# Optimization experiments

Measured on AMD Instinct MI355X. Metric: run time of the kernel, lower is better.

The kernel has to match this reference:

```python
import jax, jax.numpy as jnp
import numpy as np

N = 20000
E = 640000
D = 128
NORM_FACTOR = 100.0
LN_EPS = 1e-5


def _layer_norm(x, g, b):
    mu = jnp.mean(x, axis=-1, keepdims=True)
    var = jnp.var(x, axis=-1, keepdims=True)
    return (x - mu) * jax.lax.rsqrt(var + LN_EPS) * g + b


def setup_inputs() -> dict:
    key = jax.random.key(0)
    ks = jax.random.split(key, 16)

    def lin(k, fan_in, shape):
        bound = 1.0 / np.sqrt(fan_in)
        return jax.random.uniform(k, shape, jnp.float32, -bound, bound)

    h = jax.random.normal(ks[0], (N, D), jnp.float32)
    distances = jax.random.uniform(ks[1], (E, 1), jnp.float32)
    edges = jax.random.randint(ks[2], (2, E), 0, N, jnp.int64)
    node_mask = jnp.ones((N, 1), jnp.float32)
    edge_mask = jnp.ones((E, 1), jnp.float32)

    return {
        "h": h, "distances": distances, "node_mask": node_mask, "edge_mask": edge_mask,
        # linear: in->out
        "lin_w": lin(ks[3], D, (D, D)), "lin_b": lin(ks[4], D, (D,)),
        # att_mlp: (2D+1)->2D -> 2D->D -> D->1
        "att_w1": lin(ks[5], 2 * D + 1, (2 * D, 2 * D + 1)), "att_b1": lin(ks[5], 2 * D + 1, (2 * D,)),
        "att_w2": lin(ks[6], 2 * D, (D, 2 * D)), "att_b2": lin(ks[6], 2 * D, (D,)),
        "att_w3": lin(ks[7], D, (1, D)), "att_b3": lin(ks[7], D, (1,)),
        # node_mlp: D->D, LN, SiLU, D->D
        "nm_w1": lin(ks[8], D, (D, D)), "nm_b1": lin(ks[8], D, (D,)),
        "nm_ln_g": jnp.ones((D,), jnp.float32), "nm_ln_b": jnp.zeros((D,), jnp.float32),
        "nm_w2": lin(ks[9], D, (D, D)), "nm_b2": lin(ks[9], D, (D,)),
        # final LayerNorm
        "ln_g": jnp.ones((D,), jnp.float32), "ln_b": jnp.zeros((D,), jnp.float32),
        "edges": edges,
    }


def reference(h, distances, node_mask, edge_mask,
              lin_w, lin_b, att_w1, att_b1, att_w2, att_b2, att_w3, att_b3,
              nm_w1, nm_b1, nm_ln_g, nm_ln_b, nm_w2, nm_b2, ln_g, ln_b, edges):
    x = h @ lin_w.T + lin_b                                  # [N, D]
    row, col = edges[0], edges[1]
    x_row = x[row]                                           # [E, D]
    x_col = x[col]                                           # [E, D]

    # DenseAtt
    d = distances * edge_mask
    x_cat = jnp.concatenate([x_row, x_col, d], axis=1)       # [E, 2D+1]
    a = jax.nn.silu(x_cat @ att_w1.T + att_b1)
    a = jax.nn.silu(a @ att_w2.T + att_b2)
    att = jax.nn.sigmoid(a @ att_w3.T + att_b3) * edge_mask  # [E, 1]

    agg = x_col * att                                        # [E, D]
    out = jax.ops.segment_sum(agg, row, num_segments=N) / NORM_FACTOR

    # node_mlp + residual
    o = out @ nm_w1.T + nm_b1
    o = jax.nn.silu(_layer_norm(o, nm_ln_g, nm_ln_b))
    o = o @ nm_w2.T + nm_b2
    hh = o + x

    hh = _layer_norm(hh, ln_g, ln_b)
    hh = jax.nn.silu(hh)                                     # act = SiLU
    return hh
```

## Files before the change

### kernel.cpp

```cpp
#include <hip/hip_runtime.h>
#include <hip/hip_bf16.h>

#define N_NODES 20000
#define E_EDGES 640000
#define DIM 128
#define CAP 96
#define EPB 64
#define NPB 8
#define XST 264

typedef __attribute__((ext_vector_type(8))) short bf16x8;
typedef __attribute__((ext_vector_type(4))) float f32x4;
typedef __attribute__((ext_vector_type(2))) float f32x2;
typedef __attribute__((ext_vector_type(4))) unsigned u32x4;

#define LOG2E 1.44269504f
__device__ __forceinline__ float fsilu(float x) {
    return x * __builtin_amdgcn_rcpf(1.f + __builtin_amdgcn_exp2f(-LOG2E * x));
}
__device__ __forceinline__ float fsig(float x) {
    return __builtin_amdgcn_rcpf(1.f + __builtin_amdgcn_exp2f(-LOG2E * x));
}
__device__ __forceinline__ f32x2 fsilu2(f32x2 v) {
    f32x2 m = v * (-LOG2E);
    f32x2 e; e.x = __builtin_amdgcn_exp2f(m.x); e.y = __builtin_amdgcn_exp2f(m.y);
    f32x2 den = e + 1.0f;
    f32x2 r; r.x = __builtin_amdgcn_rcpf(den.x); r.y = __builtin_amdgcn_rcpf(den.y);
    return v * r;
}

__device__ __forceinline__ unsigned short f2bf(float x) {
    union { float f; unsigned u; } v; v.f = x;
    unsigned r = (v.u + 0x7fffu + ((v.u >> 16) & 1u)) >> 16;
    return (unsigned short)r;
}
__device__ __forceinline__ float bf2f(unsigned short s) {
    union { unsigned u; float f; } v; v.u = ((unsigned)s) << 16;
    return v.f;
}
__device__ __forceinline__ unsigned pack_bf16(float lo, float hi) {
    union { float f; unsigned u; } a, b; a.f = lo; b.f = hi;
    unsigned ul = a.u + 0x8000u, uh = b.u + 0x8000u;
    return __builtin_amdgcn_perm(uh, ul, 0x07060302u);
}

#define PRE_PREP_BLOCKS 64
#define PRE_LIN_BLOCKS  625
#define PRE_CNT_BLOCKS  2500
__global__ __launch_bounds__(256) void pre_kernel(
    const float* __restrict__ w1, const float* __restrict__ w2,
    unsigned short* __restrict__ w1b, float* __restrict__ w1p,
    unsigned short* __restrict__ w2b,
    const float* __restrict__ h, const float* __restrict__ lw,
    const float* __restrict__ lb, float* __restrict__ x,
    unsigned short* __restrict__ xb,
    const int* __restrict__ edges, int* __restrict__ cnt, int E) {
    __shared__ float hs[32][128];
    int b = blockIdx.x;
    int t = threadIdx.x;

    if (b < PRE_PREP_BLOCKS) {
        int i = b * 256 + t;
        const int stride = PRE_PREP_BLOCKS * 256;
        for (int idx = i; idx < 256 * 256; idx += stride) {
            int o = idx >> 8, k = idx & 255;
            w1b[idx] = f2bf(w1[o * 257 + k]);
        }
        for (int idx = i; idx < 128 * 256; idx += stride) {
            int n2 = idx >> 8, p = idx & 255;
            int bb = p & ~31, off = p & 31;
            int ksrc = bb + (off >> 1) + ((off & 1) << 4);
            w2b[idx] = f2bf(w2[n2 * 256 + ksrc]);
        }
        for (int idx = i; idx < 256; idx += stride) {
            int bb = idx & ~31, off = idx & 31;
            int ksrc = bb + (off >> 1) + ((off & 1) << 4);
            w1p[idx] = w1[ksrc * 257 + 256];
        }
    } else if (b < PRE_PREP_BLOCKS + PRE_LIN_BLOCKS) {
        int nb = b - PRE_PREP_BLOCKS;
        int n0 = nb * 32;
        int ch = t & 127, g = t >> 7;
#pragma unroll
        for (int j = 0; j < 16; ++j) hs[g * 16 + j][ch] = h[(size_t)(n0 + g * 16 + j) * DIM + ch];
        __syncthreads();
        float acc[16];
#pragma unroll
        for (int j = 0; j < 16; ++j) acc[j] = 0.f;
        for (int kc = 0; kc < 128; kc += 4) {
            float4 wv = *(const float4*)&lw[(size_t)ch * DIM + kc];
#pragma unroll
            for (int j = 0; j < 16; ++j) {
                float4 hv = *(const float4*)&hs[g * 16 + j][kc];
                acc[j] += wv.x * hv.x + wv.y * hv.y + wv.z * hv.z + wv.w * hv.w;
            }
        }
        float bias = lb[ch];
#pragma unroll
        for (int j = 0; j < 16; ++j) {
            float v = acc[j] + bias;
            int n = n0 + g * 16 + j;
            x[(size_t)n * DIM + ch] = v;
            xb[(size_t)n * DIM + ch] = f2bf(v);
        }
    } else {
        int e = (b - PRE_PREP_BLOCKS - PRE_LIN_BLOCKS) * 256 + t;
        if (e < E) atomicAdd(&cnt[edges[e]], 1);
    }
}

__global__ __launch_bounds__(1024) void scan_kernel(const int* __restrict__ cnt,
                                                    int* __restrict__ off) {
    __shared__ int wsum[16], wbase[16];
    int t = threadIdx.x;
    int lane = t & 63, wid = t >> 6;
    int base = t * 20;
    int loc[20];
    int s = 0;
#pragma unroll
    for (int i = 0; i < 20; ++i) {
        int idx = base + i;
        int v = 0;
        if (idx < N_NODES) { v = cnt[idx]; v = v > CAP ? CAP : v; }
        loc[i] = s; s += v;
    }
    int inc = s;
#pragma unroll
    for (int d = 1; d < 64; d <<= 1) {
        int u = __shfl_up(inc, d);
        if (lane >= d) inc += u;
    }
    if (lane == 63) wsum[wid] = inc;
    __syncthreads();
    if (t < 16) {
        int v = wsum[t];
        int inc2 = v;
#pragma unroll
        for (int d = 1; d < 16; d <<= 1) {
            int u = __shfl_up(inc2, d);
            if (t >= d) inc2 += u;
        }
        wbase[t] = inc2 - v;
        if (t == 15) off[N_NODES] = inc2;
    }
    __syncthreads();
    int ex = wbase[wid] + inc - s;
#pragma unroll
    for (int i = 0; i < 20; ++i) {
        int idx = base + i;
        if (idx < N_NODES) off[idx] = ex + loc[i];
    }
}

#define MID_PRC_BLOCKS 1250
#define MID_SCAT_BLOCKS 2500
__global__ __launch_bounds__(256) void mid_kernel(
    const unsigned short* __restrict__ xb,
    const unsigned short* __restrict__ w1b,
    const float* __restrict__ b1,
    unsigned short* __restrict__ prb, unsigned short* __restrict__ pcb,
    const int* __restrict__ edges,
    const float* __restrict__ dist, const float* __restrict__ emask,
    int* __restrict__ cnt2, const int* __restrict__ off,
    int4* __restrict__ flat, int E) {
    int b = blockIdx.x;
    if (b < MID_PRC_BLOCKS) {
        int n0 = b * 16;
        int w = threadIdx.x >> 6, lane = threadIdx.x & 63;
        int lrow = lane & 15, quad = lane >> 4;

        bf16x8 a[4];
#pragma unroll
        for (int kk = 0; kk < 4; ++kk)
            a[kk] = *(const bf16x8*)&xb[(size_t)(n0 + lrow) * DIM + kk * 32 + quad * 8];

        f32x4 z = {0.f, 0.f, 0.f, 0.f};
#pragma unroll
        for (int i = 0; i < 8; ++i) {
            int gt = w * 8 + i;
            int half = gt >> 4;
            int obase = (gt & 15) * 16;
            f32x4 acc = z;
#pragma unroll
            for (int kk = 0; kk < 4; ++kk) {
                bf16x8 bfrag = *(const bf16x8*)&w1b[(size_t)(obase + lrow) * 256 + half * 128 + kk * 32 + quad * 8];
                acc = __builtin_amdgcn_mfma_f32_16x16x32_bf16(a[kk], bfrag, acc, 0, 0, 0);
            }
            int o = obase + lrow;
            if (half == 0) {
                float bias = b1[o];
#pragma unroll
                for (int r = 0; r < 4; ++r)
                    prb[(size_t)(n0 + quad * 4 + r) * 256 + o] = f2bf(acc[r] + bias);
            } else {
#pragma unroll
                for (int r = 0; r < 4; ++r)
                    pcb[(size_t)(n0 + quad * 4 + r) * 256 + o] = f2bf(acc[r]);
            }
        }
    } else {
        int e = (b - MID_PRC_BLOCKS) * 256 + threadIdx.x;
        if (e < E) {
            int r = edges[e];
            int col = edges[E + e];
            float em = emask[e];
            float dv = dist[e] * em;
            int slot = atomicAdd(&cnt2[r], 1);
            if (slot < CAP) {
                int4 wv;
                union { float f; int i; } u1, u2; u1.f = dv; u2.f = em;
                wv.x = r; wv.y = col; wv.z = u1.i; wv.w = u2.i;
                flat[off[r] + slot] = wv;
            }
        }
    }
}

__global__ __launch_bounds__(512, 4) void edge_kernel(
    const unsigned short* __restrict__ prb, const unsigned short* __restrict__ pcb,
    int4* __restrict__ flat, const int* __restrict__ off,
    const float* __restrict__ w1p,
    const unsigned short* __restrict__ w2b, const float* __restrict__ b2,
    const float* __restrict__ w3, const float* __restrict__ b3v) {
    __shared__ unsigned short buf[EPB * XST];
    __shared__ float part[8][EPB];
    __shared__ float w1ps[256];

    int tid = threadIdx.x;
    int eb = blockIdx.x * EPB;
    int count = off[N_NODES];

    if (tid < 256) w1ps[tid] = w1p[tid];

    int ge = tid >> 3, cb = tid & 7;
    int eidx = eb + ge;
    int4 fv;
    if (eidx < count) fv = flat[eidx];
    else { fv.x = 0; fv.y = 0; fv.z = 0; fv.w = 0; }
    const unsigned short* prow = prb + (size_t)fv.x * 256 + cb * 32;
    const unsigned short* pcp  = pcb + (size_t)fv.y * 256 + cb * 32;
    union { int i; float f; } ud; ud.i = fv.z;
    float d = ud.f;

    bf16x8 pA0 = *(const bf16x8*)&prow[0];
    bf16x8 pB0 = *(const bf16x8*)&prow[16];
    bf16x8 qA0 = *(const bf16x8*)&pcp[0];
    bf16x8 qB0 = *(const bf16x8*)&pcp[16];
    bf16x8 pA1 = *(const bf16x8*)&prow[8];
    bf16x8 pB1 = *(const bf16x8*)&prow[24];
    bf16x8 qA1 = *(const bf16x8*)&pcp[8];
    bf16x8 qB1 = *(const bf16x8*)&pcp[24];

    int wave = tid >> 6, lane = tid & 63;
    int lrow = lane & 15, quad = lane >> 4;
    int n2 = wave * 16 + lrow;
    float bias2 = b2[n2];
    float w3v = w3[n2];

    __syncthreads();

    {
        const float* wp = &w1ps[cb * 32];
        f32x2 d2 = {d, d};
        unsigned u[16];
#pragma unroll
        for (int l = 0; l < 8; ++l) {
            f32x2 p = {bf2f((unsigned short)pA0[l]), bf2f((unsigned short)pB0[l])};
            f32x2 q = {bf2f((unsigned short)qA0[l]), bf2f((unsigned short)qB0[l])};
            f32x2 wv2 = *(const f32x2*)&wp[2 * l];
            f32x2 sv = fsilu2(p + q + d2 * wv2);
            u[l] = pack_bf16(sv.x, sv.y);
        }
#pragma unroll
        for (int l = 0; l < 8; ++l) {
            f32x2 p = {bf2f((unsigned short)pA1[l]), bf2f((unsigned short)pB1[l])};
            f32x2 q = {bf2f((unsigned short)qA1[l]), bf2f((unsigned short)qB1[l])};
            f32x2 wv2 = *(const f32x2*)&wp[16 + 2 * l];
            f32x2 sv = fsilu2(p + q + d2 * wv2);
            u[8 + l] = pack_bf16(sv.x, sv.y);
        }
        u32x4* w4 = (u32x4*)&buf[ge * XST + cb * 32];
        u32x4 v0 = {u[0], u[1], u[2], u[3]};
        u32x4 v1 = {u[4], u[5], u[6], u[7]};
        u32x4 v2 = {u[8], u[9], u[10], u[11]};
        u32x4 v3 = {u[12], u[13], u[14], u[15]};
        w4[0] = v0; w4[1] = v1; w4[2] = v2; w4[3] = v3;
    }
    __syncthreads();

    f32x4 zz = {0.f, 0.f, 0.f, 0.f};
    f32x4 acc2[4];
#pragma unroll
    for (int mt = 0; mt < 4; ++mt) acc2[mt] = zz;

    for (int kk = 0; kk < 8; ++kk) {
        int ka = kk * 32 + quad * 8;
        bf16x8 bfrag = *(const bf16x8*)&w2b[(size_t)n2 * 256 + ka];
#pragma unroll
        for (int mt = 0; mt < 4; ++mt) {
            bf16x8 a = *(bf16x8*)&buf[(mt * 16 + lrow) * XST + ka];
            acc2[mt] = __builtin_amdgcn_mfma_f32_16x16x32_bf16(a, bfrag, acc2[mt], 0, 0, 0);
        }
    }

    float s[4][4];
#pragma unroll
    for (int mt = 0; mt < 4; ++mt)
#pragma unroll
        for (int r = 0; r < 4; ++r)
            s[mt][r] = fsilu(acc2[mt][r] + bias2) * w3v;
#pragma unroll
    for (int off2 = 1; off2 < 16; off2 <<= 1) {
#pragma unroll
        for (int mt = 0; mt < 4; ++mt)
#pragma unroll
            for (int r = 0; r < 4; ++r)
                s[mt][r] += __shfl_xor(s[mt][r], off2);
    }
    if (lrow == 0) {
#pragma unroll
        for (int mt = 0; mt < 4; ++mt)
#pragma unroll
            for (int r = 0; r < 4; ++r)
                part[wave][mt * 16 + quad * 4 + r] = s[mt][r];
    }
    __syncthreads();

    if (tid < EPB) {
        int idx = eb + tid;
        if (idx < count) {
            float ssum = b3v[0];
#pragma unroll
            for (int w = 0; w < 8; ++w) ssum += part[w][tid];
            union { int i; float f; } ue; ue.i = flat[idx].w;
            union { float f; int i; } ua; ua.f = fsig(ssum) * ue.f;
            ((int*)&flat[idx])[3] = ua.i;
        }
    }
}

__global__ __launch_bounds__(256) void node_kernel(
    const int4* __restrict__ flat,
    const int* __restrict__ cnt, const int* __restrict__ off,
    const unsigned short* __restrict__ xb,
    const float* __restrict__ x,
    const float* __restrict__ w1, const float* __restrict__ bb1,
    const float* __restrict__ lng, const float* __restrict__ lnb,
    const float* __restrict__ w2, const float* __restrict__ bb2,
    const float* __restrict__ gF, const float* __restrict__ bF,
    float* __restrict__ out, int E) {
    __shared__ float atts[NPB][CAP];
    __shared__ int   cols[NPB][CAP];
    __shared__ float outv[NPB][128];
    __shared__ float bufs[NPB][128];
    __shared__ float mu_s[NPB], rs_s[NPB];
    __shared__ int cnts[NPB];

    int t = threadIdx.x;
    int n0 = blockIdx.x * NPB;

    if (t < NPB) { int c = cnt[n0 + t]; cnts[t] = c > CAP ? CAP : c; }
    __syncthreads();

    {
        int jg = t >> 5, l = t & 31;
        int c = cnts[jg];
        const int4* fl = flat + off[n0 + jg];
        for (int i = l; i < c; i += 32) {
            int4 v = fl[i];
            union { int i; float f; } ua; ua.i = v.w;
            atts[jg][i] = ua.f;
            cols[jg][i] = v.y;
        }
    }
    __syncthreads();

    int w = t >> 6, lane = t & 63;
    int islot = lane >> 4;
    int co = lane & 15;
#pragma unroll
    for (int jj = 0; jj < 2; ++jj) {
        int j = w * 2 + jj;
        int c = cnts[j];
        float acc[8];
#pragma unroll
        for (int k = 0; k < 8; ++k) acc[k] = 0.f;
        for (int base = 0; base < c; base += 8) {
            int i0 = base + islot, i1 = base + 4 + islot;
            bool k0 = i0 < c, k1 = i1 < c;
            int c0 = cols[j][k0 ? i0 : 0];
            int c1 = cols[j][k1 ? i1 : 0];
            float a0 = k0 ? atts[j][i0] : 0.f;
            float a1 = k1 ? atts[j][i1] : 0.f;
            bf16x8 q0 = *(const bf16x8*)&xb[(size_t)c0 * DIM + co * 8];
            bf16x8 q1 = *(const bf16x8*)&xb[(size_t)c1 * DIM + co * 8];
#pragma unroll
            for (int k = 0; k < 8; ++k) acc[k] += a0 * bf2f((unsigned short)q0[k]);
#pragma unroll
            for (int k = 0; k < 8; ++k) acc[k] += a1 * bf2f((unsigned short)q1[k]);
        }
#pragma unroll
        for (int k = 0; k < 8; ++k) {
            acc[k] += __shfl_xor(acc[k], 16);
            acc[k] += __shfl_xor(acc[k], 32);
        }
        if (islot == 0) {
            float4 v0 = {acc[0] * 0.01f, acc[1] * 0.01f, acc[2] * 0.01f, acc[3] * 0.01f};
            float4 v1 = {acc[4] * 0.01f, acc[5] * 0.01f, acc[6] * 0.01f, acc[7] * 0.01f};
            *(float4*)&outv[j][co * 8] = v0;
            *(float4*)&outv[j][co * 8 + 4] = v1;
        }
    }
    __syncthreads();

    int h = t >> 7, ch = t & 127;
    float xres[4];
#pragma unroll
    for (int jj = 0; jj < 4; ++jj)
        xres[jj] = x[(size_t)(n0 + h * 4 + jj) * DIM + ch];

    float a1[4] = {0, 0, 0, 0};
    for (int kc = 0; kc < 128; kc += 4) {
        float4 wv = *(const float4*)&w1[(size_t)ch * DIM + kc];
#pragma unroll
        for (int jj = 0; jj < 4; ++jj) {
            int j = h * 4 + jj;
            float4 ov = *(const float4*)&outv[j][kc];
            a1[jj] += wv.x * ov.x + wv.y * ov.y + wv.z * ov.z + wv.w * ov.w;
        }
    }
    float bias1 = bb1[ch];
#pragma unroll
    for (int jj = 0; jj < 4; ++jj) bufs[h * 4 + jj][ch] = a1[jj] + bias1;
    __syncthreads();

    {
        int j = t >> 5, l = t & 31;
        float s = 0.f, qq = 0.f;
#pragma unroll
        for (int i = 0; i < 4; ++i) { float v = bufs[j][l + 32 * i]; s += v; qq += v * v; }
#pragma unroll
        for (int off2 = 16; off2; off2 >>= 1) { s += __shfl_xor(s, off2); qq += __shfl_xor(qq, off2); }
        if (l == 0) {
            float mu = s * (1.f / 128.f);
            float var = qq * (1.f / 128.f) - mu * mu;
            mu_s[j] = mu; rs_s[j] = __builtin_amdgcn_rsqf(var + 1e-5f);
        }
    }
    __syncthreads();

    float g = lng[ch], bb = lnb[ch];
    float h2[4];
#pragma unroll
    for (int jj = 0; jj < 4; ++jj) {
        int j = h * 4 + jj;
        h2[jj] = fsilu((bufs[j][ch] - mu_s[j]) * rs_s[j] * g + bb);
    }
    __syncthreads();
#pragma unroll
    for (int jj = 0; jj < 4; ++jj) bufs[h * 4 + jj][ch] = h2[jj];
    __syncthreads();

    float a3[4] = {0, 0, 0, 0};
    for (int kc = 0; kc < 128; kc += 4) {
        float4 wv = *(const float4*)&w2[(size_t)ch * DIM + kc];
#pragma unroll
        for (int jj = 0; jj < 4; ++jj) {
            int j = h * 4 + jj;
            float4 bv = *(const float4*)&bufs[j][kc];
            a3[jj] += wv.x * bv.x + wv.y * bv.y + wv.z * bv.z + wv.w * bv.w;
        }
    }
    float bias2 = bb2[ch];
    float hh[4];
#pragma unroll
    for (int jj = 0; jj < 4; ++jj) hh[jj] = a3[jj] + bias2 + xres[jj];
    __syncthreads();
#pragma unroll
    for (int jj = 0; jj < 4; ++jj) bufs[h * 4 + jj][ch] = hh[jj];
    __syncthreads();

    {
        int j = t >> 5, l = t & 31;
        float s = 0.f, qq = 0.f;
#pragma unroll
        for (int i = 0; i < 4; ++i) { float v = bufs[j][l + 32 * i]; s += v; qq += v * v; }
#pragma unroll
        for (int off2 = 16; off2; off2 >>= 1) { s += __shfl_xor(s, off2); qq += __shfl_xor(qq, off2); }
        if (l == 0) {
            float mu = s * (1.f / 128.f);
            float var = qq * (1.f / 128.f) - mu * mu;
            mu_s[j] = mu; rs_s[j] = __builtin_amdgcn_rsqf(var + 1e-5f);
        }
    }
    __syncthreads();

    float gf = gF[ch], bf = bF[ch];
#pragma unroll
    for (int jj = 0; jj < 4; ++jj) {
        int j = h * 4 + jj;
        float y = (hh[jj] - mu_s[j]) * rs_s[j] * gf + bf;
        out[(size_t)(n0 + j) * DIM + ch] = fsilu(y);
    }
}

extern "C" void kernel_launch(void* const* d_in, const int* in_sizes, int n_in,
                              void* d_out, int out_size, void* d_ws, size_t ws_size,
                              hipStream_t stream) {
    const float* h         = (const float*)d_in[0];
    const float* distances = (const float*)d_in[1];
    const float* edge_mask = (const float*)d_in[3];
    const float* lin_w     = (const float*)d_in[4];
    const float* lin_b     = (const float*)d_in[5];
    const float* att_w1    = (const float*)d_in[6];
    const float* att_b1    = (const float*)d_in[7];
    const float* att_w2    = (const float*)d_in[8];
    const float* att_b2    = (const float*)d_in[9];
    const float* att_w3    = (const float*)d_in[10];
    const float* att_b3    = (const float*)d_in[11];
    const float* nm_w1     = (const float*)d_in[12];
    const float* nm_b1     = (const float*)d_in[13];
    const float* nm_ln_g   = (const float*)d_in[14];
    const float* nm_ln_b   = (const float*)d_in[15];
    const float* nm_w2     = (const float*)d_in[16];
    const float* nm_b2     = (const float*)d_in[17];
    const float* ln_g      = (const float*)d_in[18];
    const float* ln_b      = (const float*)d_in[19];
    const int*   edges     = (const int*)d_in[20];
    float* out = (float*)d_out;

    const int N = N_NODES, E = E_EDGES;

    char* ws = (char*)d_ws;
    float* x            = (float*)ws;            ws += (size_t)N * DIM * 4;
    unsigned short* xb  = (unsigned short*)ws;   ws += (size_t)N * DIM * 2;
    int* cnt            = (int*)ws;              ws += (size_t)N * 4;
    int* cnt2           = (int*)ws;              ws += (size_t)N * 4;
    int* off            = (int*)ws;              ws += (size_t)(N + 4) * 4;
    int4* flat          = (int4*)ws;             ws += (size_t)E * 16;
    unsigned short* w1b = (unsigned short*)ws;   ws += 256 * 256 * 2;
    float* w1p          = (float*)ws;            ws += 256 * 4;
    unsigned short* w2b = (unsigned short*)ws;   ws += 128 * 256 * 2;
    unsigned short* prb = (unsigned short*)ws;   ws += (size_t)N * 256 * 2;
    unsigned short* pcb = (unsigned short*)ws;   ws += (size_t)N * 256 * 2;

    hipMemsetAsync(cnt, 0, (size_t)N * 8, stream);

    pre_kernel<<<PRE_PREP_BLOCKS + PRE_LIN_BLOCKS + PRE_CNT_BLOCKS, 256, 0, stream>>>(
        att_w1, att_w2, w1b, w1p, w2b,
        h, lin_w, lin_b, x, xb,
        edges, cnt, E);
    scan_kernel<<<1, 1024, 0, stream>>>(cnt, off);
    mid_kernel<<<MID_PRC_BLOCKS + MID_SCAT_BLOCKS, 256, 0, stream>>>(
        xb, w1b, att_b1, prb, pcb, edges, distances, edge_mask, cnt2, off, flat, E);
    edge_kernel<<<E / EPB, 512, 0, stream>>>(prb, pcb, flat, off,
                                             w1p, w2b, att_b2, att_w3, att_b3);
    node_kernel<<<N / NPB, 256, 0, stream>>>(flat, cnt, off, xb, x,
                                             nm_w1, nm_b1, nm_ln_g, nm_ln_b,
                                             nm_w2, nm_b2, ln_g, ln_b, out, E);
}
```

Before: 441.2 us.

## Replace CSR scan and flat edge scatter with fixed-capacity adjacency lists

Drops the single-block scan kernel and the second counting/scatter pass. Edges are now written directly into a per-node fixed-capacity (CAP) adjacency array holding edge id and column. The edge kernel processes edges in original order, reads indices and distances directly, and writes attention values to a separate per-edge array. The node kernel gathers attention through the edge id. This removes a serialized launch and a pass over the edges, at the cost of an indirect attention gather and padded adjacency storage.

```diff
diff --git a/kernel.cpp b/kernel.cpp
--- a/kernel.cpp
+++ b/kernel.cpp
@@ -46,7 +46,7 @@
 
 #define PRE_PREP_BLOCKS 64
 #define PRE_LIN_BLOCKS  625
-#define PRE_CNT_BLOCKS  2500
+#define PRE_ADJ_BLOCKS  2500
 __global__ __launch_bounds__(256) void pre_kernel(
     const float* __restrict__ w1, const float* __restrict__ w2,
     unsigned short* __restrict__ w1b, float* __restrict__ w1p,
@@ -54,7 +54,8 @@
     const float* __restrict__ h, const float* __restrict__ lw,
     const float* __restrict__ lb, float* __restrict__ x,
     unsigned short* __restrict__ xb,
-    const int* __restrict__ edges, int* __restrict__ cnt, int E) {
+    const int* __restrict__ edges, int* __restrict__ cnt,
+    int2* __restrict__ adj2, int E) {
     __shared__ float hs[32][128];
     int b = blockIdx.x;
     int t = threadIdx.x;
@@ -105,142 +106,80 @@
         }
     } else {
         int e = (b - PRE_PREP_BLOCKS - PRE_LIN_BLOCKS) * 256 + t;
-        if (e < E) atomicAdd(&cnt[edges[e]], 1);
-    }
-}
-
-__global__ __launch_bounds__(1024) void scan_kernel(const int* __restrict__ cnt,
-                                                    int* __restrict__ off) {
-    __shared__ int wsum[16], wbase[16];
-    int t = threadIdx.x;
-    int lane = t & 63, wid = t >> 6;
-    int base = t * 20;
-    int loc[20];
-    int s = 0;
-#pragma unroll
-    for (int i = 0; i < 20; ++i) {
-        int idx = base + i;
-        int v = 0;
-        if (idx < N_NODES) { v = cnt[idx]; v = v > CAP ? CAP : v; }
-        loc[i] = s; s += v;
-    }
-    int inc = s;
-#pragma unroll
-    for (int d = 1; d < 64; d <<= 1) {
-        int u = __shfl_up(inc, d);
-        if (lane >= d) inc += u;
-    }
-    if (lane == 63) wsum[wid] = inc;
-    __syncthreads();
-    if (t < 16) {
-        int v = wsum[t];
-        int inc2 = v;
-#pragma unroll
-        for (int d = 1; d < 16; d <<= 1) {
-            int u = __shfl_up(inc2, d);
-            if (t >= d) inc2 += u;
-        }
-        wbase[t] = inc2 - v;
-        if (t == 15) off[N_NODES] = inc2;
-    }
-    __syncthreads();
-    int ex = wbase[wid] + inc - s;
-#pragma unroll
-    for (int i = 0; i < 20; ++i) {
-        int idx = base + i;
-        if (idx < N_NODES) off[idx] = ex + loc[i];
-    }
-}
-
-#define MID_PRC_BLOCKS 1250
-#define MID_SCAT_BLOCKS 2500
-__global__ __launch_bounds__(256) void mid_kernel(
+        if (e < E) {
+            int r = edges[e];
+            int col = edges[E + e];
+            int slot = atomicAdd(&cnt[r], 1);
+            if (slot < CAP) { int2 v; v.x = e; v.y = col; adj2[(size_t)r * CAP + slot] = v; }
+        }
+    }
+}
+
+#define PRC_NPB 16
+__global__ __launch_bounds__(256) void prc_kernel(
     const unsigned short* __restrict__ xb,
     const unsigned short* __restrict__ w1b,
     const float* __restrict__ b1,
-    unsigned short* __restrict__ prb, unsigned short* __restrict__ pcb,
-    const int* __restrict__ edges,
-    const float* __restrict__ dist, const float* __restrict__ emask,
-    int* __restrict__ cnt2, const int* __restrict__ off,
-    int4* __restrict__ flat, int E) {
-    int b = blockIdx.x;
-    if (b < MID_PRC_BLOCKS) {
-        int n0 = b * 16;
-        int w = threadIdx.x >> 6, lane = threadIdx.x & 63;
-        int lrow = lane & 15, quad = lane >> 4;
-
-        bf16x8 a[4];
-#pragma unroll
-        for (int kk = 0; kk < 4; ++kk)
-            a[kk] = *(const bf16x8*)&xb[(size_t)(n0 + lrow) * DIM + kk * 32 + quad * 8];
-
-        f32x4 z = {0.f, 0.f, 0.f, 0.f};
-#pragma unroll
-        for (int i = 0; i < 8; ++i) {
-            int gt = w * 8 + i;
-            int half = gt >> 4;
-            int obase = (gt & 15) * 16;
-            f32x4 acc = z;
-#pragma unroll
-            for (int kk = 0; kk < 4; ++kk) {
-                bf16x8 bfrag = *(const bf16x8*)&w1b[(size_t)(obase + lrow) * 256 + half * 128 + kk * 32 + quad * 8];
-                acc = __builtin_amdgcn_mfma_f32_16x16x32_bf16(a[kk], bfrag, acc, 0, 0, 0);
-            }
-            int o = obase + lrow;
-            if (half == 0) {
-                float bias = b1[o];
-#pragma unroll
-                for (int r = 0; r < 4; ++r)
-                    prb[(size_t)(n0 + quad * 4 + r) * 256 + o] = f2bf(acc[r] + bias);
-            } else {
-#pragma unroll
-                for (int r = 0; r < 4; ++r)
-                    pcb[(size_t)(n0 + quad * 4 + r) * 256 + o] = f2bf(acc[r]);
-            }
-        }
-    } else {
-        int e = (b - MID_PRC_BLOCKS) * 256 + threadIdx.x;
-        if (e < E) {
-            int r = edges[e];
-            int col = edges[E + e];
-            float em = emask[e];
-            float dv = dist[e] * em;
-            int slot = atomicAdd(&cnt2[r], 1);
-            if (slot < CAP) {
-                int4 wv;
-                union { float f; int i; } u1, u2; u1.f = dv; u2.f = em;
-                wv.x = r; wv.y = col; wv.z = u1.i; wv.w = u2.i;
-                flat[off[r] + slot] = wv;
-            }
+    unsigned short* __restrict__ prb, unsigned short* __restrict__ pcb) {
+    int n0 = blockIdx.x * PRC_NPB;
+    int w = threadIdx.x >> 6, lane = threadIdx.x & 63;
+    int lrow = lane & 15, quad = lane >> 4;
+
+    bf16x8 a[4];
+#pragma unroll
+    for (int kk = 0; kk < 4; ++kk)
+        a[kk] = *(const bf16x8*)&xb[(size_t)(n0 + lrow) * DIM + kk * 32 + quad * 8];
+
+    f32x4 z = {0.f, 0.f, 0.f, 0.f};
+#pragma unroll
+    for (int i = 0; i < 8; ++i) {
+        int gt = w * 8 + i;
+        int half = gt >> 4;
+        int obase = (gt & 15) * 16;
+        f32x4 acc = z;
+#pragma unroll
+        for (int kk = 0; kk < 4; ++kk) {
+            bf16x8 bfrag = *(const bf16x8*)&w1b[(size_t)(obase + lrow) * 256 + half * 128 + kk * 32 + quad * 8];
+            acc = __builtin_amdgcn_mfma_f32_16x16x32_bf16(a[kk], bfrag, acc, 0, 0, 0);
+        }
+        int o = obase + lrow;
+        if (half == 0) {
+            float bias = b1[o];
+#pragma unroll
+            for (int r = 0; r < 4; ++r)
+                prb[(size_t)(n0 + quad * 4 + r) * 256 + o] = f2bf(acc[r] + bias);
+        } else {
+#pragma unroll
+            for (int r = 0; r < 4; ++r)
+                pcb[(size_t)(n0 + quad * 4 + r) * 256 + o] = f2bf(acc[r]);
         }
     }
 }
 
 __global__ __launch_bounds__(512, 4) void edge_kernel(
     const unsigned short* __restrict__ prb, const unsigned short* __restrict__ pcb,
-    int4* __restrict__ flat, const int* __restrict__ off,
+    const float* __restrict__ dist, const float* __restrict__ emask,
+    const int* __restrict__ edges,
     const float* __restrict__ w1p,
     const unsigned short* __restrict__ w2b, const float* __restrict__ b2,
-    const float* __restrict__ w3, const float* __restrict__ b3v) {
+    const float* __restrict__ w3, const float* __restrict__ b3v,
+    float* __restrict__ attv, int E) {
     __shared__ unsigned short buf[EPB * XST];
     __shared__ float part[8][EPB];
     __shared__ float w1ps[256];
 
     int tid = threadIdx.x;
     int eb = blockIdx.x * EPB;
-    int count = off[N_NODES];
 
     if (tid < 256) w1ps[tid] = w1p[tid];
 
     int ge = tid >> 3, cb = tid & 7;
-    int eidx = eb + ge;
-    int4 fv;
-    if (eidx < count) fv = flat[eidx];
-    else { fv.x = 0; fv.y = 0; fv.z = 0; fv.w = 0; }
-    const unsigned short* prow = prb + (size_t)fv.x * 256 + cb * 32;
-    const unsigned short* pcp  = pcb + (size_t)fv.y * 256 + cb * 32;
-    union { int i; float f; } ud; ud.i = fv.z;
-    float d = ud.f;
+    int e = eb + ge;
+    int r = edges[e];
+    int c2 = edges[E + e];
+    float d = dist[e] * emask[e];
+    const unsigned short* prow = prb + (size_t)r * 256 + cb * 32;
+    const unsigned short* pcp  = pcb + (size_t)c2 * 256 + cb * 32;
 
     bf16x8 pA0 = *(const bf16x8*)&prow[0];
     bf16x8 pB0 = *(const bf16x8*)&prow[16];
@@ -307,41 +246,36 @@
 #pragma unroll
     for (int mt = 0; mt < 4; ++mt)
 #pragma unroll
-        for (int r = 0; r < 4; ++r)
-            s[mt][r] = fsilu(acc2[mt][r] + bias2) * w3v;
+        for (int r2 = 0; r2 < 4; ++r2)
+            s[mt][r2] = fsilu(acc2[mt][r2] + bias2) * w3v;
 #pragma unroll
     for (int off2 = 1; off2 < 16; off2 <<= 1) {
 #pragma unroll
         for (int mt = 0; mt < 4; ++mt)
 #pragma unroll
-            for (int r = 0; r < 4; ++r)
-                s[mt][r] += __shfl_xor(s[mt][r], off2);
+            for (int r2 = 0; r2 < 4; ++r2)
+                s[mt][r2] += __shfl_xor(s[mt][r2], off2);
     }
     if (lrow == 0) {
 #pragma unroll
         for (int mt = 0; mt < 4; ++mt)
 #pragma unroll
-            for (int r = 0; r < 4; ++r)
-                part[wave][mt * 16 + quad * 4 + r] = s[mt][r];
+            for (int r2 = 0; r2 < 4; ++r2)
+                part[wave][mt * 16 + quad * 4 + r2] = s[mt][r2];
     }
     __syncthreads();
 
     if (tid < EPB) {
-        int idx = eb + tid;
-        if (idx < count) {
-            float ssum = b3v[0];
-#pragma unroll
-            for (int w = 0; w < 8; ++w) ssum += part[w][tid];
-            union { int i; float f; } ue; ue.i = flat[idx].w;
-            union { float f; int i; } ua; ua.f = fsig(ssum) * ue.f;
-            ((int*)&flat[idx])[3] = ua.i;
-        }
+        float ssum = b3v[0];
+#pragma unroll
+        for (int w = 0; w < 8; ++w) ssum += part[w][tid];
+        attv[eb + tid] = fsig(ssum) * emask[eb + tid];
     }
 }
 
 __global__ __launch_bounds__(256) void node_kernel(
-    const int4* __restrict__ flat,
-    const int* __restrict__ cnt, const int* __restrict__ off,
+    const float* __restrict__ attv, const int2* __restrict__ adj2,
+    const int* __restrict__ cnt,
     const unsigned short* __restrict__ xb,
     const float* __restrict__ x,
     const float* __restrict__ w1, const float* __restrict__ bb1,
@@ -365,11 +299,10 @@
     {
         int jg = t >> 5, l = t & 31;
         int c = cnts[jg];
-        const int4* fl = flat + off[n0 + jg];
+        const int2* al = adj2 + (size_t)(n0 + jg) * CAP;
         for (int i = l; i < c; i += 32) {
-            int4 v = fl[i];
-            union { int i; float f; } ua; ua.i = v.w;
-            atts[jg][i] = ua.f;
+            int2 v = al[i];
+            atts[jg][i] = attv[v.x];
             cols[jg][i] = v.y;
         }
     }
@@ -535,27 +468,25 @@
     float* x            = (float*)ws;            ws += (size_t)N * DIM * 4;
     unsigned short* xb  = (unsigned short*)ws;   ws += (size_t)N * DIM * 2;
     int* cnt            = (int*)ws;              ws += (size_t)N * 4;
-    int* cnt2           = (int*)ws;              ws += (size_t)N * 4;
-    int* off            = (int*)ws;              ws += (size_t)(N + 4) * 4;
-    int4* flat          = (int4*)ws;             ws += (size_t)E * 16;
+    int2* adj2          = (int2*)ws;             ws += (size_t)N * CAP * 8;
+    float* attv         = (float*)ws;            ws += (size_t)E * 4;
     unsigned short* w1b = (unsigned short*)ws;   ws += 256 * 256 * 2;
     float* w1p          = (float*)ws;            ws += 256 * 4;
     unsigned short* w2b = (unsigned short*)ws;   ws += 128 * 256 * 2;
     unsigned short* prb = (unsigned short*)ws;   ws += (size_t)N * 256 * 2;
     unsigned short* pcb = (unsigned short*)ws;   ws += (size_t)N * 256 * 2;
 
-    hipMemsetAsync(cnt, 0, (size_t)N * 8, stream);
-
-    pre_kernel<<<PRE_PREP_BLOCKS + PRE_LIN_BLOCKS + PRE_CNT_BLOCKS, 256, 0, stream>>>(
+    hipMemsetAsync(cnt, 0, (size_t)N * 4, stream);
+
+    pre_kernel<<<PRE_PREP_BLOCKS + PRE_LIN_BLOCKS + PRE_ADJ_BLOCKS, 256, 0, stream>>>(
         att_w1, att_w2, w1b, w1p, w2b,
         h, lin_w, lin_b, x, xb,
-        edges, cnt, E);
-    scan_kernel<<<1, 1024, 0, stream>>>(cnt, off);
-    mid_kernel<<<MID_PRC_BLOCKS + MID_SCAT_BLOCKS, 256, 0, stream>>>(
-        xb, w1b, att_b1, prb, pcb, edges, distances, edge_mask, cnt2, off, flat, E);
-    edge_kernel<<<E / EPB, 512, 0, stream>>>(prb, pcb, flat, off,
-                                             w1p, w2b, att_b2, att_w3, att_b3);
-    node_kernel<<<N / NPB, 256, 0, stream>>>(flat, cnt, off, xb, x,
+        edges, cnt, adj2, E);
+    prc_kernel<<<N / PRC_NPB, 256, 0, stream>>>(xb, w1b, att_b1, prb, pcb);
+    edge_kernel<<<E / EPB, 512, 0, stream>>>(prb, pcb, distances, edge_mask, edges,
+                                             w1p, w2b, att_b2,
+                                             att_w3, att_b3, attv, E);
+    node_kernel<<<N / NPB, 256, 0, stream>>>(attv, adj2, cnt, xb, x,
                                              nm_w1, nm_b1, nm_ln_g, nm_ln_b,
                                              nm_w2, nm_b2, ln_g, ln_b, out, E);
 }
```

After: 410.1 us. 1.08x faster.
